# Kernel tuning notes

Measured on AMD Instinct MI355X. Metric: run time of the kernel, lower is better.

The kernel has to match this reference:

```python
import jax, jax.numpy as jnp
import numpy as np

B, C, H, W = 32, 3, 480, 640
_GRAY_W = jnp.array([0.299, 0.587, 0.114], dtype=jnp.float32)  # torchvision rgb_to_grayscale weights


def _blend(img1, img2, ratio):
    # torchvision _blend for float images: clamp to [0, 1]
    return jnp.clip(ratio * img1 + (1.0 - ratio) * img2, 0.0, 1.0)


def _rgb_to_gray(x):
    # x: [B,3,H,W] -> [B,1,H,W]
    return jnp.einsum('bchw,c->bhw', x, _GRAY_W)[:, None]


def _adjust_hue(x, hf):
    # x: [B,3,H,W] in [0,1], hf: [B] hue shift. RGB->HSV, h += hf (mod 1), HSV->RGB.
    r, g, b = x[:, 0], x[:, 1], x[:, 2]
    maxc = jnp.max(x, axis=1)
    minc = jnp.min(x, axis=1)
    v = maxc
    cr = maxc - minc
    eqc = cr == 0
    crd = jnp.where(eqc, 1.0, cr)
    s = cr / jnp.where(maxc == 0, 1.0, maxc)
    rc = (maxc - r) / crd
    gc = (maxc - g) / crd
    bc = (maxc - b) / crd
    hr = jnp.where(maxc == r, bc - gc, 0.0)
    hg = jnp.where((maxc == g) & (maxc != r), 2.0 + rc - bc, 0.0)
    hb = jnp.where((maxc != g) & (maxc != r), 4.0 + gc - rc, 0.0)
    h = ((hr + hg + hb) / 6.0) % 1.0
    h = (h + hf[:, None, None]) % 1.0
    # HSV -> RGB
    i6 = h * 6.0
    i = jnp.floor(i6)
    f = i6 - i
    i = i.astype(jnp.int32) % 6
    p = v * (1.0 - s)
    q = v * (1.0 - f * s)
    t = v * (1.0 - (1.0 - f) * s)

    def sel(a0, a1, a2, a3, a4, a5):
        return jnp.select([i == 0, i == 1, i == 2, i == 3, i == 4], [a0, a1, a2, a3, a4], a5)

    r2 = sel(v, q, p, p, t, v)
    g2 = sel(t, v, v, q, p, p)
    b2 = sel(p, p, t, v, v, q)
    return jnp.stack([r2, g2, b2], axis=1)


def setup_inputs() -> dict:
    key = jax.random.key(0)
    k0, k1, k2, k3, k4 = jax.random.split(key, 5)
    x = jax.random.uniform(k0, (B, C, H, W), dtype=jnp.float32)
    brightness_f = jax.random.uniform(k1, (B,), minval=0.7, maxval=1.3, dtype=jnp.float32)
    contrast_f = jax.random.uniform(k2, (B,), minval=0.7, maxval=1.3, dtype=jnp.float32)
    saturation_f = jax.random.uniform(k3, (B,), minval=0.7, maxval=1.3, dtype=jnp.float32)
    hue_f = jax.random.uniform(k4, (B,), minval=-0.3, maxval=0.3, dtype=jnp.float32)
    return {"x": x, "brightness_f": brightness_f, "contrast_f": contrast_f,
            "saturation_f": saturation_f, "hue_f": hue_f, "num_samples": 1}


def reference(x, brightness_f, contrast_f, saturation_f, hue_f, num_samples):
    # Replicate each image num_samples times along batch -> [B*N, 3, H, W]
    x = jnp.repeat(x, num_samples, axis=0)
    bf = brightness_f[:, None, None, None]
    cf = contrast_f[:, None, None, None]
    sf = saturation_f[:, None, None, None]
    # brightness: blend with zeros
    x = jnp.clip(x * bf, 0.0, 1.0)
    # contrast: blend with per-image mean of grayscale
    gray = _rgb_to_gray(x)
    mean = jnp.mean(gray, axis=(2, 3), keepdims=True)
    x = _blend(x, mean, cf)
    # saturation: blend with grayscale of current image
    x = _blend(x, _rgb_to_gray(x), sf)
    # hue shift via HSV roundtrip
    x = _adjust_hue(x, hue_f)
    return x
```

## Files before the change

kernel.cpp:

```cpp
#include <hip/hip_runtime.h>

#define HW      307200
#define HW4     76800
#define CHW     921600
#define RED_BPB 60
#define APP_BPB 300

typedef float vfloat4 __attribute__((ext_vector_type(4)));

struct RGB { float r, g, b; };

__global__ __launch_bounds__(256) void cr_reduce_gray(
    const float* __restrict__ x,
    const float* __restrict__ bright,
    float* __restrict__ part_ws,
    int ns)
{
    int b   = blockIdx.x / RED_BPB;
    int blk = blockIdx.x % RED_BPB;
    int b_in = (ns == 1) ? b : (b / ns);

    const vfloat4* rp = (const vfloat4*)(x + (size_t)b_in * CHW);
    const vfloat4* gp = rp + HW4;
    const vfloat4* bp = gp + HW4;
    float bf = bright[b];

    float acc = 0.0f;
    #pragma unroll
    for (int it = 0; it < 5; ++it) {
        int p = blk * 256 + threadIdx.x + it * (RED_BPB * 256);
        vfloat4 r  = rp[p];
        vfloat4 g  = gp[p];
        vfloat4 bl = bp[p];
        #pragma unroll
        for (int k = 0; k < 4; ++k) {
            float rr = fminf(fmaxf(r[k]  * bf, 0.0f), 1.0f);
            float gg = fminf(fmaxf(g[k]  * bf, 0.0f), 1.0f);
            float bb = fminf(fmaxf(bl[k] * bf, 0.0f), 1.0f);
            acc += 0.299f * rr + 0.587f * gg + 0.114f * bb;
        }
    }

    #pragma unroll
    for (int off = 32; off > 0; off >>= 1)
        acc += __shfl_down(acc, off);

    __shared__ float wsum[4];
    int lane = threadIdx.x & 63;
    int wave = threadIdx.x >> 6;
    if (lane == 0) wsum[wave] = acc;
    __syncthreads();
    if (threadIdx.x == 0)
        part_ws[b * RED_BPB + blk] = wsum[0] + wsum[1] + wsum[2] + wsum[3];
}

__device__ __forceinline__ RGB cr_process(
    float r, float g, float b,
    float bf, float cf, float sf, float hf, float cmean)
{
    r = fminf(fmaxf(r * bf, 0.0f), 1.0f);
    g = fminf(fmaxf(g * bf, 0.0f), 1.0f);
    b = fminf(fmaxf(b * bf, 0.0f), 1.0f);
    r = fminf(fmaxf(cf * r + cmean, 0.0f), 1.0f);
    g = fminf(fmaxf(cf * g + cmean, 0.0f), 1.0f);
    b = fminf(fmaxf(cf * b + cmean, 0.0f), 1.0f);
    float gray = 0.299f * r + 0.587f * g + 0.114f * b;
    float oms = (1.0f - sf) * gray;
    r = fminf(fmaxf(sf * r + oms, 0.0f), 1.0f);
    g = fminf(fmaxf(sf * g + oms, 0.0f), 1.0f);
    b = fminf(fmaxf(sf * b + oms, 0.0f), 1.0f);

    float maxc = fmaxf(r, fmaxf(g, b));
    float minc = fminf(r, fminf(g, b));
    float v  = maxc;
    float cr = maxc - minc;
    float crd = (cr == 0.0f) ? 1.0f : cr;
    float invcrd = 1.0f / crd;
    float md = (maxc == 0.0f) ? 1.0f : maxc;
    float s = cr / md;
    float rc = (maxc - r) * invcrd;
    float gc = (maxc - g) * invcrd;
    float bc = (maxc - b) * invcrd;

    float h = (maxc == r) ? (bc - gc)
            : ((maxc == g) ? (2.0f + rc - bc)
                           : (4.0f + gc - rc));
    h = h * (1.0f / 6.0f);
    h = h - floorf(h);
    h = h + hf;
    h = h - floorf(h);

    float i6 = h * 6.0f;
    float fi = floorf(i6);
    float f  = i6 - fi;
    int i = ((int)fi) % 6;

    float p = v * (1.0f - s);
    float q = v * (1.0f - f * s);
    float t = v * (1.0f - (1.0f - f) * s);

    RGB o;
    o.r = (i == 0 || i == 5) ? v : (i == 1 ? q : (i == 4 ? t : p));
    o.g = (i == 1 || i == 2) ? v : (i == 0 ? t : (i == 3 ? q : p));
    o.b = (i == 3 || i == 4) ? v : (i == 5 ? q : (i == 2 ? t : p));
    return o;
}

__global__ __launch_bounds__(256) void cr_apply(
    const float* __restrict__ x,
    const float* __restrict__ bright,
    const float* __restrict__ contrast,
    const float* __restrict__ sat,
    const float* __restrict__ hue,
    const float* __restrict__ part_ws,
    float* __restrict__ out,
    int ns)
{
    int b    = blockIdx.x / APP_BPB;
    int pblk = blockIdx.x % APP_BPB;
    int p4   = pblk * 256 + threadIdx.x;
    int b_in = (ns == 1) ? b : (b / ns);

    __shared__ float smean;
    if (threadIdx.x < 64) {
        float v = (threadIdx.x < RED_BPB) ? part_ws[b * RED_BPB + threadIdx.x] : 0.0f;
        #pragma unroll
        for (int off = 32; off > 0; off >>= 1)
            v += __shfl_down(v, off);
        if (threadIdx.x == 0) smean = v * (1.0f / (float)HW);
    }
    __syncthreads();

    const vfloat4* rp = (const vfloat4*)(x + (size_t)b_in * CHW);
    const vfloat4* gp = rp + HW4;
    const vfloat4* bp = gp + HW4;
    vfloat4* orp = (vfloat4*)(out + (size_t)b * CHW);
    vfloat4* ogp = orp + HW4;
    vfloat4* obp = ogp + HW4;

    float bf = bright[b];
    float cf = contrast[b];
    float sf = sat[b];
    float hf = hue[b];
    float cmean = (1.0f - cf) * smean;

    vfloat4 r  = rp[p4];
    vfloat4 g  = gp[p4];
    vfloat4 bl = bp[p4];
    vfloat4 ro, go, bo;

    #pragma unroll
    for (int k = 0; k < 4; ++k) {
        RGB o = cr_process(r[k], g[k], bl[k], bf, cf, sf, hf, cmean);
        ro[k] = o.r;
        go[k] = o.g;
        bo[k] = o.b;
    }

    __builtin_nontemporal_store(ro, &orp[p4]);
    __builtin_nontemporal_store(go, &ogp[p4]);
    __builtin_nontemporal_store(bo, &obp[p4]);
}

extern "C" void kernel_launch(void* const* d_in, const int* in_sizes, int n_in,
                              void* d_out, int out_size, void* d_ws, size_t ws_size,
                              hipStream_t stream) {
    const float* x  = (const float*)d_in[0];
    const float* bf = (const float*)d_in[1];
    const float* cf = (const float*)d_in[2];
    const float* sf = (const float*)d_in[3];
    const float* hf = (const float*)d_in[4];
    float* out = (float*)d_out;

    int ns = out_size / in_sizes[0];
    if (ns < 1) ns = 1;
    int B_out = out_size / CHW;

    float* part_ws = (float*)d_ws;

    cr_reduce_gray<<<dim3(B_out * RED_BPB), dim3(256), 0, stream>>>(
        x, bf, part_ws, ns);

    cr_apply<<<dim3(B_out * APP_BPB), dim3(256), 0, stream>>>(
        x, bf, cf, sf, hf, part_ws, out, ns);
}
```

Before: 227.0 us.

## Fuse reduction and apply into one cooperative kernel with grid sync

```diff
diff --git a/kernel.cpp b/kernel.cpp
--- a/kernel.cpp
+++ b/kernel.cpp
@@ -1,58 +1,17 @@
 #include <hip/hip_runtime.h>
+#include <hip/hip_cooperative_groups.h>
+
+namespace cg = cooperative_groups;
 
 #define HW      307200
 #define HW4     76800
 #define CHW     921600
-#define RED_BPB 60
-#define APP_BPB 300
+#define BPB     30
+#define GPT     10
 
 typedef float vfloat4 __attribute__((ext_vector_type(4)));
 
 struct RGB { float r, g, b; };
-
-__global__ __launch_bounds__(256) void cr_reduce_gray(
-    const float* __restrict__ x,
-    const float* __restrict__ bright,
-    float* __restrict__ part_ws,
-    int ns)
-{
-    int b   = blockIdx.x / RED_BPB;
-    int blk = blockIdx.x % RED_BPB;
-    int b_in = (ns == 1) ? b : (b / ns);
-
-    const vfloat4* rp = (const vfloat4*)(x + (size_t)b_in * CHW);
-    const vfloat4* gp = rp + HW4;
-    const vfloat4* bp = gp + HW4;
-    float bf = bright[b];
-
-    float acc = 0.0f;
-    #pragma unroll
-    for (int it = 0; it < 5; ++it) {
-        int p = blk * 256 + threadIdx.x + it * (RED_BPB * 256);
-        vfloat4 r  = rp[p];
-        vfloat4 g  = gp[p];
-        vfloat4 bl = bp[p];
-        #pragma unroll
-        for (int k = 0; k < 4; ++k) {
-            float rr = fminf(fmaxf(r[k]  * bf, 0.0f), 1.0f);
-            float gg = fminf(fmaxf(g[k]  * bf, 0.0f), 1.0f);
-            float bb = fminf(fmaxf(bl[k] * bf, 0.0f), 1.0f);
-            acc += 0.299f * rr + 0.587f * gg + 0.114f * bb;
-        }
-    }
-
-    #pragma unroll
-    for (int off = 32; off > 0; off >>= 1)
-        acc += __shfl_down(acc, off);
-
-    __shared__ float wsum[4];
-    int lane = threadIdx.x & 63;
-    int wave = threadIdx.x >> 6;
-    if (lane == 0) wsum[wave] = acc;
-    __syncthreads();
-    if (threadIdx.x == 0)
-        part_ws[b * RED_BPB + blk] = wsum[0] + wsum[1] + wsum[2] + wsum[3];
-}
 
 __device__ __forceinline__ RGB cr_process(
     float r, float g, float b,
@@ -106,24 +65,60 @@
     return o;
 }
 
-__global__ __launch_bounds__(256) void cr_apply(
+__global__ __launch_bounds__(256) void cr_fused(
     const float* __restrict__ x,
     const float* __restrict__ bright,
     const float* __restrict__ contrast,
     const float* __restrict__ sat,
     const float* __restrict__ hue,
-    const float* __restrict__ part_ws,
+    float* __restrict__ part_ws,
     float* __restrict__ out,
     int ns)
 {
-    int b    = blockIdx.x / APP_BPB;
-    int pblk = blockIdx.x % APP_BPB;
-    int p4   = pblk * 256 + threadIdx.x;
+    int b   = blockIdx.x / BPB;
+    int blk = blockIdx.x % BPB;
     int b_in = (ns == 1) ? b : (b / ns);
+    int base = blk * (256 * GPT) + threadIdx.x;
 
+    const vfloat4* rp = (const vfloat4*)(x + (size_t)b_in * CHW);
+    const vfloat4* gp = rp + HW4;
+    const vfloat4* bp = gp + HW4;
+
+    float bf = bright[b];
+
+    float acc = 0.0f;
+    #pragma unroll
+    for (int it = 0; it < GPT; ++it) {
+        int p = base + it * 256;
+        vfloat4 r  = rp[p];
+        vfloat4 g  = gp[p];
+        vfloat4 bl = bp[p];
+        #pragma unroll
+        for (int k = 0; k < 4; ++k) {
+            float rr = fminf(fmaxf(r[k]  * bf, 0.0f), 1.0f);
+            float gg = fminf(fmaxf(g[k]  * bf, 0.0f), 1.0f);
+            float bb = fminf(fmaxf(bl[k] * bf, 0.0f), 1.0f);
+            acc += 0.299f * rr + 0.587f * gg + 0.114f * bb;
+        }
+    }
+
+    #pragma unroll
+    for (int off = 32; off > 0; off >>= 1)
+        acc += __shfl_down(acc, off);
+
+    __shared__ float wsum[4];
     __shared__ float smean;
+    int lane = threadIdx.x & 63;
+    int wave = threadIdx.x >> 6;
+    if (lane == 0) wsum[wave] = acc;
+    __syncthreads();
+    if (threadIdx.x == 0)
+        part_ws[b * BPB + blk] = wsum[0] + wsum[1] + wsum[2] + wsum[3];
+
+    cg::this_grid().sync();
+
     if (threadIdx.x < 64) {
-        float v = (threadIdx.x < RED_BPB) ? part_ws[b * RED_BPB + threadIdx.x] : 0.0f;
+        float v = (threadIdx.x < BPB) ? part_ws[b * BPB + threadIdx.x] : 0.0f;
         #pragma unroll
         for (int off = 32; off > 0; off >>= 1)
             v += __shfl_down(v, off);
@@ -131,35 +126,33 @@
     }
     __syncthreads();
 
-    const vfloat4* rp = (const vfloat4*)(x + (size_t)b_in * CHW);
-    const vfloat4* gp = rp + HW4;
-    const vfloat4* bp = gp + HW4;
-    vfloat4* orp = (vfloat4*)(out + (size_t)b * CHW);
-    vfloat4* ogp = orp + HW4;
-    vfloat4* obp = ogp + HW4;
-
-    float bf = bright[b];
     float cf = contrast[b];
     float sf = sat[b];
     float hf = hue[b];
     float cmean = (1.0f - cf) * smean;
 
-    vfloat4 r  = rp[p4];
-    vfloat4 g  = gp[p4];
-    vfloat4 bl = bp[p4];
-    vfloat4 ro, go, bo;
+    vfloat4* orp = (vfloat4*)(out + (size_t)b * CHW);
+    vfloat4* ogp = orp + HW4;
+    vfloat4* obp = ogp + HW4;
 
-    #pragma unroll
-    for (int k = 0; k < 4; ++k) {
-        RGB o = cr_process(r[k], g[k], bl[k], bf, cf, sf, hf, cmean);
-        ro[k] = o.r;
-        go[k] = o.g;
-        bo[k] = o.b;
+    #pragma unroll 2
+    for (int it = 0; it < GPT; ++it) {
+        int p = base + it * 256;
+        vfloat4 r  = rp[p];
+        vfloat4 g  = gp[p];
+        vfloat4 bl = bp[p];
+        vfloat4 ro, go, bo;
+        #pragma unroll
+        for (int k = 0; k < 4; ++k) {
+            RGB o = cr_process(r[k], g[k], bl[k], bf, cf, sf, hf, cmean);
+            ro[k] = o.r;
+            go[k] = o.g;
+            bo[k] = o.b;
+        }
+        __builtin_nontemporal_store(ro, &orp[p]);
+        __builtin_nontemporal_store(go, &ogp[p]);
+        __builtin_nontemporal_store(bo, &obp[p]);
     }
-
-    __builtin_nontemporal_store(ro, &orp[p4]);
-    __builtin_nontemporal_store(go, &ogp[p4]);
-    __builtin_nontemporal_store(bo, &obp[p4]);
 }
 
 extern "C" void kernel_launch(void* const* d_in, const int* in_sizes, int n_in,
@@ -178,9 +171,9 @@
 
     float* part_ws = (float*)d_ws;
 
-    cr_reduce_gray<<<dim3(B_out * RED_BPB), dim3(256), 0, stream>>>(
-        x, bf, part_ws, ns);
-
-    cr_apply<<<dim3(B_out * APP_BPB), dim3(256), 0, stream>>>(
-        x, bf, cf, sf, hf, part_ws, out, ns);
+    void* args[] = { (void*)&x, (void*)&bf, (void*)&cf, (void*)&sf, (void*)&hf,
+                     (void*)&part_ws, (void*)&out, (void*)&ns };
+    hipLaunchCooperativeKernel((void*)cr_fused,
+                               dim3(B_out * BPB), dim3(256),
+                               args, 0, stream);
 }
```

Result: slower. 347.0 us (+52.8%).
